# Kernel tuning notes

Hardware: AMD Instinct MI355X
Metric: run time of the kernel (lower is better)

Reference implementation:

```python
import jax, jax.numpy as jnp
import numpy as np

B, S, C, H = 2, 4096, 512, 8
D = C // H  # per-head depth


def setup_inputs() -> dict:
    key = jax.random.key(0)
    ks = jax.random.split(key, 12)
    scale = 1.0 / np.sqrt(C)
    inp = {
        "q": jax.random.normal(ks[0], (B, S, C), jnp.float32),
        "k": jax.random.normal(ks[1], (B, S, C), jnp.float32),
        "v": jax.random.normal(ks[2], (B, S, C), jnp.float32),
        "mask": jax.random.randint(ks[3], (1, 1, S, S), 0, 2).astype(jnp.float32),
        "wq": jax.random.normal(ks[4], (C, C), jnp.float32) * scale,
        "bq": jnp.zeros((C,), jnp.float32),
        "wk": jax.random.normal(ks[5], (C, C), jnp.float32) * scale,
        "bk": jnp.zeros((C,), jnp.float32),
        "wv": jax.random.normal(ks[6], (C, C), jnp.float32) * scale,
        "bv": jnp.zeros((C,), jnp.float32),
        "wo": jax.random.normal(ks[7], (C, C), jnp.float32) * scale,
        "bo": jnp.zeros((C,), jnp.float32),
    }
    return inp


def _split_heads(x):
    # [B,S,C] -> [B,H,S,D]
    b, s, _ = x.shape
    return x.reshape(b, s, H, D).transpose(0, 2, 1, 3)


def reference(q, k, v, mask, wq, bq, wk, bk, wv, bv, wo, bo):
    # torch Linear: y = x @ W.T + b
    qh = _split_heads(q @ wq.T + bq)  # [B,H,S,D]
    kh = _split_heads(k @ wk.T + bk)
    vh = _split_heads(v @ wv.T + bv)

    # scaled dot-product attention with additive legacy mask
    scores = jnp.einsum("bhqd,bhkd->bhqk", qh, kh) / jnp.sqrt(jnp.float32(D))
    scores = scores + mask * jnp.float32(-1e12)
    attn = jax.nn.softmax(scores, axis=-1)  # [B,H,Sq,Sk]
    out_h = jnp.einsum("bhqk,bhkd->bhqd", attn, vh)  # [B,H,S,D]

    # merge heads and output projection
    concat = out_h.transpose(0, 2, 1, 3).reshape(q.shape[0], -1, C)
    out = concat @ wo.T + bo  # [B,S,C]
    return out, attn
```

## Files before the change

### kernel.cpp

```cpp
#include <hip/hip_runtime.h>
#include <hip/hip_bf16.h>
#include <cstdint>

#define SB 4096
#define CB 512
#define HB 8
#define DB 64
#define BB 2

#define QSCALE 0.18033688011112042f

typedef __attribute__((ext_vector_type(8))) short s16x8;
typedef __attribute__((ext_vector_type(4))) short s16x4;
typedef __attribute__((ext_vector_type(4))) float f32x4;

__device__ __forceinline__ short f2bf(float f) {
    union { float f; unsigned int u; } v; v.f = f;
    unsigned int r = v.u + 0x7fffu + ((v.u >> 16) & 1u);
    return (short)(r >> 16);
}

__device__ __forceinline__ unsigned int cvtpk(float lo, float hi) {
    unsigned int r;
    asm("v_cvt_pk_bf16_f32 %0, %1, %2" : "=v"(r) : "v"(lo), "v"(hi));
    return r;
}

__device__ __forceinline__ f32x4 mfma16(s16x8 a, s16x8 b, f32x4 c) {
    return __builtin_amdgcn_mfma_f32_16x16x32_bf16(a, b, c, 0, 0, 0);
}

__device__ __forceinline__ f32x4 mfma16x16(s16x4 a, s16x4 b, f32x4 c) {
    asm("v_mfma_f32_16x16x16_bf16 %0, %1, %2, %0" : "+v"(c) : "v"(a), "v"(b));
    return c;
}

__global__ __launch_bounds__(256) void qkv_proj_kernel(
    const float* __restrict__ q, const float* __restrict__ k, const float* __restrict__ v,
    const float* __restrict__ wq, const float* __restrict__ wk, const float* __restrict__ wv,
    const float* __restrict__ bq, const float* __restrict__ bk, const float* __restrict__ bv,
    unsigned short* __restrict__ Qh, unsigned short* __restrict__ Kh,
    unsigned short* __restrict__ Vt)
{
    const int z = blockIdx.z;
    const float* X = (z == 0) ? q : (z == 1) ? k : v;
    const float* W = (z == 0) ? wq : (z == 1) ? wk : wv;
    const float* bias = (z == 0) ? bq : (z == 1) ? bk : bv;
    unsigned short* dst = (z == 0) ? Qh : (z == 1) ? Kh : Vt;
    const float oscale = (z == 0) ? QSCALE : 1.0f;
    const int which = (z == 2) ? 2 : 0;

    __shared__ __align__(16) short As[128 * 40];
    __shared__ __align__(16) short Bs[64 * 40];
    const int t = threadIdx.x;
    const int w = t >> 6, lane = t & 63, g = lane >> 4, c = lane & 15;
    const int wr = w >> 1, wc = w & 1;
    const int m0 = blockIdx.x * 128, n0 = blockIdx.y * 64;

    f32x4 acc[4][2];
#pragma unroll
    for (int i = 0; i < 4; ++i)
#pragma unroll
        for (int j = 0; j < 2; ++j) acc[i][j] = (f32x4){0.f, 0.f, 0.f, 0.f};

    for (int k0 = 0; k0 < CB; k0 += 32) {
        __syncthreads();
#pragma unroll
        for (int i = 0; i < 4; ++i) {
            int idx = t + i * 256; int r = idx >> 3, c4 = idx & 7;
            float4 vv = *(const float4*)(X + (size_t)(m0 + r) * CB + k0 + c4 * 4);
            s16x4 p; p[0] = f2bf(vv.x); p[1] = f2bf(vv.y); p[2] = f2bf(vv.z); p[3] = f2bf(vv.w);
            *(s16x4*)&As[r * 40 + c4 * 4] = p;
        }
#pragma unroll
        for (int i = 0; i < 2; ++i) {
            int idx = t + i * 256; int r = idx >> 3, c4 = idx & 7;
            float4 vv = *(const float4*)(W + (size_t)(n0 + r) * CB + k0 + c4 * 4);
            s16x4 p; p[0] = f2bf(vv.x); p[1] = f2bf(vv.y); p[2] = f2bf(vv.z); p[3] = f2bf(vv.w);
            *(s16x4*)&Bs[r * 40 + c4 * 4] = p;
        }
        __syncthreads();
        const int koff = g * 8;
        s16x8 a[4], bb[2];
#pragma unroll
        for (int mf = 0; mf < 4; ++mf)
            a[mf] = *(const s16x8*)&As[(wr * 64 + mf * 16 + c) * 40 + koff];
#pragma unroll
        for (int nf = 0; nf < 2; ++nf)
            bb[nf] = *(const s16x8*)&Bs[(wc * 32 + nf * 16 + c) * 40 + koff];
#pragma unroll
        for (int mf = 0; mf < 4; ++mf)
#pragma unroll
            for (int nf = 0; nf < 2; ++nf)
                acc[mf][nf] = mfma16(a[mf], bb[nf], acc[mf][nf]);
    }

#pragma unroll
    for (int nf = 0; nf < 2; ++nf) {
        const int n = n0 + wc * 32 + nf * 16 + c;
        const float bv2 = bias[n];
        const int h = n >> 6, d = n & 63;
#pragma unroll
        for (int mf = 0; mf < 4; ++mf) {
#pragma unroll
            for (int r = 0; r < 4; ++r) {
                int m = m0 + wr * 64 + mf * 16 + g * 4 + r;
                float val = (acc[mf][nf][r] + bv2) * oscale;
                int b = m >> 12, s = m & (SB - 1);
                size_t off;
                if (which == 0) off = (((size_t)(b * HB + h)) * SB + s) * DB + d;
                else            off = (((size_t)(b * HB + h)) * DB + d) * SB + s;
                dst[off] = (unsigned short)f2bf(val);
            }
        }
    }
}

__global__ __launch_bounds__(256) void maskbits_kernel(
    const float* __restrict__ mask, unsigned long long* __restrict__ bits)
{
    size_t idx = (size_t)blockIdx.x * 256 + threadIdx.x;
    float v = mask[idx];
    unsigned long long b = __ballot(v != 0.0f);
    if ((threadIdx.x & 63) == 0) bits[idx >> 6] = b;
}

__global__ __launch_bounds__(512) void flash_kernel(
    const unsigned short* __restrict__ Qh, const unsigned short* __restrict__ Kh,
    const unsigned short* __restrict__ Vt, const unsigned long long* __restrict__ mbits,
    unsigned short* __restrict__ concat, float* __restrict__ invbuf)
{
    __shared__ __align__(16) short Klds[2][64 * 64];
    __shared__ __align__(16) short Vlds[2][64 * 64];

    const int t = threadIdx.x, w = t >> 6, lane = t & 63, g = lane >> 4, c = lane & 15;
    const int bid = blockIdx.x;
    const int xcd = bid & 7, idx = bid >> 3;
    const int bh = xcd * 2 + (idx >> 5);
    const int qb = idx & 31;
    const int b = bh >> 3, h = bh & 7;
    const int i0 = qb * 128;

    const unsigned short* Qbase = Qh + ((size_t)bh * SB + i0 + w * 16) * DB;
    const unsigned short* Kbase = Kh + (size_t)bh * SB * DB;
    const unsigned short* Vbase = Vt + (size_t)bh * DB * SB;

    s16x8 qf[2];
#pragma unroll
    for (int ks = 0; ks < 2; ++ks)
        qf[ks] = *(const s16x8*)(Qbase + (size_t)c * DB + ks * 32 + g * 8);

    const int qrow = i0 + w * 16 + c;
    const size_t mrowbase = (size_t)qrow * (SB / 64);
    float rowacc = 0.f;
    f32x4 acc[4];
#pragma unroll
    for (int df = 0; df < 4; ++df) acc[df] = (f32x4){0.f, 0.f, 0.f, 0.f};

    const int sr = t >> 3;
    const int colb = (t & 7) * 16;
    const int swz = (sr & 7) << 4;

    s16x8 kreg, vreg;

    auto LOAD = [&](int j0) {
        kreg = *(const s16x8*)((const char*)(Kbase + (size_t)(j0 + sr) * DB) + colb);
        vreg = *(const s16x8*)((const char*)(Vbase + (size_t)sr * SB + j0) + colb);
    };
    auto STORE = [&](int buf) {
        *(s16x8*)((char*)&Klds[buf][0] + sr * 128 + (colb ^ swz)) = kreg;
        *(s16x8*)((char*)&Vlds[buf][0] + sr * 128 + (colb ^ swz)) = vreg;
    };
    auto COMPUTE = [&](int buf, unsigned long long mw64) {
        f32x4 sc[4];
        __builtin_amdgcn_s_setprio(1);
#pragma unroll
        for (int jf = 0; jf < 4; ++jf) {
            sc[jf] = (f32x4){0.f, 0.f, 0.f, 0.f};
#pragma unroll
            for (int ks = 0; ks < 2; ++ks) {
                s16x8 kf = *(const s16x8*)((char*)&Klds[buf][0] + (jf * 16 + c) * 128 +
                                           ((ks * 64 + g * 16) ^ ((c & 7) << 4)));
                sc[jf] = mfma16(kf, qf[ks], sc[jf]);
            }
        }
        __builtin_amdgcn_s_setprio(0);

        const unsigned long long mw = mw64 >> (g * 4);
        const unsigned int nib[4] = {
            (unsigned int)mw & 0xFu, (unsigned int)(mw >> 16) & 0xFu,
            (unsigned int)(mw >> 32) & 0xFu, (unsigned int)(mw >> 48) & 0xFu };

        s16x4 pf4[4];
#pragma unroll
        for (int jf = 0; jf < 4; ++jf) {
            float e[4];
#pragma unroll
            for (int r = 0; r < 4; ++r)
                e[r] = ((nib[jf] >> r) & 1u) ? 0.f : __builtin_amdgcn_exp2f(sc[jf][r]);
            rowacc += (e[0] + e[1]) + (e[2] + e[3]);
            union { unsigned int u[2]; s16x4 v; } pk;
            pk.u[0] = cvtpk(e[0], e[1]);
            pk.u[1] = cvtpk(e[2], e[3]);
            pf4[jf] = pk.v;
        }

        __builtin_amdgcn_s_setprio(1);
#pragma unroll
        for (int df = 0; df < 4; ++df) {
#pragma unroll
            for (int jf = 0; jf < 4; ++jf) {
                s16x4 vf = *(const s16x4*)((char*)&Vlds[buf][0] + (df * 16 + c) * 128 +
                                           ((jf * 32 + g * 8) ^ ((c & 7) << 4)));
                acc[df] = mfma16x16(pf4[jf], vf, acc[df]);
            }
        }
        __builtin_amdgcn_s_setprio(0);
    };

    unsigned long long mwcur = mbits[mrowbase];
    LOAD(0);
    STORE(0);
    __syncthreads();
    int cur = 0;
    for (int jt = 0; jt < SB / 64 - 1; ++jt) {
        LOAD((jt + 1) * 64);
        unsigned long long mwnext = mbits[mrowbase + jt + 1];
        COMPUTE(cur, mwcur);
        STORE(cur ^ 1);
        __syncthreads();
        mwcur = mwnext;
        cur ^= 1;
    }
    COMPUTE(cur, mwcur);

    rowacc += __shfl_xor(rowacc, 16);
    rowacc += __shfl_xor(rowacc, 32);
    const float inv = 1.0f / rowacc;
    if (lane < 16) invbuf[(size_t)bh * SB + i0 + w * 16 + c] = inv;

    float ir[4];
#pragma unroll
    for (int r = 0; r < 4; ++r) ir[r] = __shfl(inv, g * 4 + r);

#pragma unroll
    for (int df = 0; df < 4; ++df) {
#pragma unroll
        for (int r = 0; r < 4; ++r) {
            const int s_ = i0 + w * 16 + g * 4 + r;
            concat[(size_t)(b * SB + s_) * CB + h * DB + df * 16 + c] =
                (unsigned short)f2bf(acc[df][r] * ir[r]);
        }
    }
}

__global__ __launch_bounds__(256) void attn_write_kernel(
    const unsigned short* __restrict__ Qh, const unsigned short* __restrict__ Kh,
    const unsigned long long* __restrict__ mbits, const float* __restrict__ invbuf,
    float* __restrict__ attnO)
{
    __shared__ __align__(16) float TP[4][16 * 64];

    const int t = threadIdx.x, w = t >> 6, lane = t & 63, g = lane >> 4, c = lane & 15;
    const int q0 = blockIdx.x * 64;
    const int ks0 = blockIdx.y * 512 + w * 128;
    const size_t bh = blockIdx.z;
    const unsigned short* Qb_ = Qh + (bh * SB + q0) * DB;
    const unsigned short* Kb_ = Kh + bh * SB * DB;
    float* aO = attnO + bh * (size_t)SB * SB;
    char* tp = (char*)&TP[w][0];

    s16x8 qf[4][2];
    float invv[4];
    size_t mrb[4];
#pragma unroll
    for (int qi = 0; qi < 4; ++qi) {
#pragma unroll
        for (int ks = 0; ks < 2; ++ks)
            qf[qi][ks] = *(const s16x8*)(Qb_ + (size_t)(qi * 16 + c) * DB + ks * 32 + g * 8);
        invv[qi] = invbuf[bh * SB + q0 + qi * 16 + c];
        mrb[qi] = (size_t)(q0 + qi * 16 + c) * (SB / 64);
    }

#pragma unroll
    for (int kc = 0; kc < 2; ++kc) {
        const int kch = ks0 + kc * 64;
        s16x8 kf[4][2];
#pragma unroll
        for (int jf = 0; jf < 4; ++jf)
#pragma unroll
            for (int ks = 0; ks < 2; ++ks)
                kf[jf][ks] = *(const s16x8*)(Kb_ + (size_t)(kch + jf * 16 + c) * DB + ks * 32 + g * 8);

#pragma unroll
        for (int qi = 0; qi < 4; ++qi) {
            f32x4 sc[4];
#pragma unroll
            for (int jf = 0; jf < 4; ++jf) {
                sc[jf] = (f32x4){0.f, 0.f, 0.f, 0.f};
#pragma unroll
                for (int ks = 0; ks < 2; ++ks)
                    sc[jf] = mfma16(kf[jf][ks], qf[qi][ks], sc[jf]);
            }
            unsigned long long mw = mbits[mrb[qi] + (kch >> 6)] >> (g * 4);
            const unsigned int nib[4] = {
                (unsigned int)mw & 0xFu, (unsigned int)(mw >> 16) & 0xFu,
                (unsigned int)(mw >> 32) & 0xFu, (unsigned int)(mw >> 48) & 0xFu };
            const float iv = invv[qi];

#pragma unroll
            for (int jf = 0; jf < 4; ++jf) {
                f32x4 o;
#pragma unroll
                for (int r = 0; r < 4; ++r)
                    o[r] = ((nib[jf] >> r) & 1u) ? 0.f : __builtin_amdgcn_exp2f(sc[jf][r]) * iv;
                *(f32x4*)(tp + c * 256 + ((jf * 64 + g * 16) ^ (c << 4))) = o;
            }

            const size_t gbase = (size_t)(q0 + qi * 16) * SB + kch;
#pragma unroll
            for (int i = 0; i < 4; ++i) {
                const int rr = i * 4 + g;
                f32x4 vv = *(const f32x4*)(tp + rr * 256 + ((c * 16) ^ (rr << 4)));
                __builtin_nontemporal_store(vv, (f32x4*)(aO + gbase + (size_t)rr * SB + c * 4));
            }
        }
    }
}

__global__ __launch_bounds__(256) void final_kernel(
    const unsigned short* __restrict__ Ain, const float* __restrict__ W,
    const float* __restrict__ bias, float* __restrict__ out)
{
    __shared__ __align__(16) short As[128 * 40];
    __shared__ __align__(16) short Bs[64 * 40];
    const int t = threadIdx.x;
    const int w = t >> 6, lane = t & 63, g = lane >> 4, c = lane & 15;
    const int wr = w >> 1, wc = w & 1;
    const int m0 = blockIdx.x * 128, n0 = blockIdx.y * 64;

    f32x4 acc[4][2];
#pragma unroll
    for (int i = 0; i < 4; ++i)
#pragma unroll
        for (int j = 0; j < 2; ++j) acc[i][j] = (f32x4){0.f, 0.f, 0.f, 0.f};

    for (int k0 = 0; k0 < CB; k0 += 32) {
        __syncthreads();
#pragma unroll
        for (int i = 0; i < 2; ++i) {
            int idx = t + i * 256; int r = idx >> 2, ch = idx & 3;
            *(s16x8*)&As[r * 40 + ch * 8] =
                *(const s16x8*)(Ain + (size_t)(m0 + r) * CB + k0 + ch * 8);
        }
#pragma unroll
        for (int i = 0; i < 2; ++i) {
            int idx = t + i * 256; int r = idx >> 3, c4 = idx & 7;
            float4 v = *(const float4*)(W + (size_t)(n0 + r) * CB + k0 + c4 * 4);
            s16x4 p; p[0] = f2bf(v.x); p[1] = f2bf(v.y); p[2] = f2bf(v.z); p[3] = f2bf(v.w);
            *(s16x4*)&Bs[r * 40 + c4 * 4] = p;
        }
        __syncthreads();
        const int koff = g * 8;
        s16x8 a[4], bb[2];
#pragma unroll
        for (int mf = 0; mf < 4; ++mf)
            a[mf] = *(const s16x8*)&As[(wr * 64 + mf * 16 + c) * 40 + koff];
#pragma unroll
        for (int nf = 0; nf < 2; ++nf)
            bb[nf] = *(const s16x8*)&Bs[(wc * 32 + nf * 16 + c) * 40 + koff];
#pragma unroll
        for (int mf = 0; mf < 4; ++mf)
#pragma unroll
            for (int nf = 0; nf < 2; ++nf)
                acc[mf][nf] = mfma16(a[mf], bb[nf], acc[mf][nf]);
    }

#pragma unroll
    for (int nf = 0; nf < 2; ++nf) {
        const int n = n0 + wc * 32 + nf * 16 + c;
        const float bv = bias[n];
#pragma unroll
        for (int mf = 0; mf < 4; ++mf) {
#pragma unroll
            for (int r = 0; r < 4; ++r) {
                int m = m0 + wr * 64 + mf * 16 + g * 4 + r;
                out[(size_t)m * CB + n] = acc[mf][nf][r] + bv;
            }
        }
    }
}

extern "C" void kernel_launch(void* const* d_in, const int* in_sizes, int n_in,
                              void* d_out, int out_size, void* d_ws, size_t ws_size,
                              hipStream_t stream) {
    const float* q    = (const float*)d_in[0];
    const float* k    = (const float*)d_in[1];
    const float* v    = (const float*)d_in[2];
    const float* mask = (const float*)d_in[3];
    const float* wq   = (const float*)d_in[4];
    const float* bq   = (const float*)d_in[5];
    const float* wk   = (const float*)d_in[6];
    const float* bk   = (const float*)d_in[7];
    const float* wv   = (const float*)d_in[8];
    const float* bv   = (const float*)d_in[9];
    const float* wo   = (const float*)d_in[10];
    const float* bo   = (const float*)d_in[11];

    const size_t NE = (size_t)BB * HB * SB * DB;
    unsigned short* Qh     = (unsigned short*)d_ws;
    unsigned short* Kh     = Qh + NE;
    unsigned short* Vt     = Kh + NE;
    unsigned short* concat = Vt + NE;
    unsigned long long* mbits = (unsigned long long*)((char*)d_ws + 4 * NE * sizeof(unsigned short));
    float* invbuf = (float*)((char*)d_ws + 4 * NE * sizeof(unsigned short) + (size_t)SB * SB / 8);

    float* outp  = (float*)d_out;
    float* attnp = outp + (size_t)BB * SB * CB;

    qkv_proj_kernel<<<dim3(64, 8, 3), 256, 0, stream>>>(q, k, v, wq, wk, wv, bq, bk, bv,
                                                        Qh, Kh, Vt);
    maskbits_kernel<<<dim3((SB * SB) / 256, 1, 1), 256, 0, stream>>>(mask, mbits);
    flash_kernel<<<dim3(512, 1, 1), 512, 0, stream>>>(Qh, Kh, Vt, mbits, concat, invbuf);
    final_kernel<<<dim3(64, 8, 1), 256, 0, stream>>>(concat, wo, bo, outp);
    attn_write_kernel<<<dim3(SB / 64, 8, HB * BB), 256, 0, stream>>>(Qh, Kh, mbits, invbuf, attnp);
}
```

Before: 434.9 us.

## Merge mask packing into QKV launch and output projection into attention write

Folds the mask-bit packing kernel into the QKV projection launch as extra z-slices, and folds the output projection GEMM into the attention-probability write kernel as an extra z-slice. This cuts the launch count from five to three, and lets independent work share the GPU at the same time. It also removes the s_setprio hints in the flash kernel and switches the large attention-matrix stores from nontemporal to regular stores. That could change cache behavior for the 512MB attention output.

Measured after the change: 485.4 us. +11.6%, slower.

```diff
diff --git a/kernel.cpp b/kernel.cpp
--- a/kernel.cpp
+++ b/kernel.cpp
@@ -35,14 +35,24 @@
     return c;
 }
 
-__global__ __launch_bounds__(256) void qkv_proj_kernel(
+__global__ __launch_bounds__(256) void qkv_mask_kernel(
     const float* __restrict__ q, const float* __restrict__ k, const float* __restrict__ v,
     const float* __restrict__ wq, const float* __restrict__ wk, const float* __restrict__ wv,
     const float* __restrict__ bq, const float* __restrict__ bk, const float* __restrict__ bv,
     unsigned short* __restrict__ Qh, unsigned short* __restrict__ Kh,
-    unsigned short* __restrict__ Vt)
+    unsigned short* __restrict__ Vt,
+    const float* __restrict__ mask, unsigned long long* __restrict__ bits)
 {
     const int z = blockIdx.z;
+    if (z >= 3) {
+        size_t idx = (((size_t)(z - 3) * 512) + blockIdx.y * 64 + blockIdx.x) * 256
+                     + threadIdx.x;
+        float mv = mask[idx];
+        unsigned long long bmask = __ballot(mv != 0.0f);
+        if ((threadIdx.x & 63) == 0) bits[idx >> 6] = bmask;
+        return;
+    }
+
     const float* X = (z == 0) ? q : (z == 1) ? k : v;
     const float* W = (z == 0) ? wq : (z == 1) ? wk : wv;
     const float* bias = (z == 0) ? bq : (z == 1) ? bk : bv;
@@ -114,15 +124,6 @@
             }
         }
     }
-}
-
-__global__ __launch_bounds__(256) void maskbits_kernel(
-    const float* __restrict__ mask, unsigned long long* __restrict__ bits)
-{
-    size_t idx = (size_t)blockIdx.x * 256 + threadIdx.x;
-    float v = mask[idx];
-    unsigned long long b = __ballot(v != 0.0f);
-    if ((threadIdx.x & 63) == 0) bits[idx >> 6] = b;
 }
 
 __global__ __launch_bounds__(512) void flash_kernel(
@@ -173,7 +174,6 @@
     };
     auto COMPUTE = [&](int buf, unsigned long long mw64) {
         f32x4 sc[4];
-        __builtin_amdgcn_s_setprio(1);
 #pragma unroll
         for (int jf = 0; jf < 4; ++jf) {
             sc[jf] = (f32x4){0.f, 0.f, 0.f, 0.f};
@@ -184,7 +184,6 @@
                 sc[jf] = mfma16(kf, qf[ks], sc[jf]);
             }
         }
-        __builtin_amdgcn_s_setprio(0);
 
         const unsigned long long mw = mw64 >> (g * 4);
         const unsigned int nib[4] = {
@@ -205,7 +204,6 @@
             pf4[jf] = pk.v;
         }
 
-        __builtin_amdgcn_s_setprio(1);
 #pragma unroll
         for (int df = 0; df < 4; ++df) {
 #pragma unroll
@@ -215,7 +213,6 @@
                 acc[df] = mfma16x16(pf4[jf], vf, acc[df]);
             }
         }
-        __builtin_amdgcn_s_setprio(0);
     };
 
     unsigned long long mwcur = mbits[mrowbase];
@@ -254,11 +251,74 @@
     }
 }
 
-__global__ __launch_bounds__(256) void attn_write_kernel(
+__global__ __launch_bounds__(256) void attn_final_kernel(
     const unsigned short* __restrict__ Qh, const unsigned short* __restrict__ Kh,
     const unsigned long long* __restrict__ mbits, const float* __restrict__ invbuf,
-    float* __restrict__ attnO)
+    float* __restrict__ attnO,
+    const unsigned short* __restrict__ Ain, const float* __restrict__ W,
+    const float* __restrict__ bias, float* __restrict__ out)
 {
+    if (blockIdx.z == 16) {
+        __shared__ __align__(16) short As[128 * 40];
+        __shared__ __align__(16) short Bs[64 * 40];
+        const int t = threadIdx.x;
+        const int w = t >> 6, lane = t & 63, g = lane >> 4, c = lane & 15;
+        const int wr = w >> 1, wc = w & 1;
+        const int m0 = blockIdx.x * 128, n0 = blockIdx.y * 64;
+
+        f32x4 acc[4][2];
+#pragma unroll
+        for (int i = 0; i < 4; ++i)
+#pragma unroll
+            for (int j = 0; j < 2; ++j) acc[i][j] = (f32x4){0.f, 0.f, 0.f, 0.f};
+
+        for (int k0 = 0; k0 < CB; k0 += 32) {
+            __syncthreads();
+#pragma unroll
+            for (int i = 0; i < 2; ++i) {
+                int idx = t + i * 256; int r = idx >> 2, ch = idx & 3;
+                *(s16x8*)&As[r * 40 + ch * 8] =
+                    *(const s16x8*)(Ain + (size_t)(m0 + r) * CB + k0 + ch * 8);
+            }
+#pragma unroll
+            for (int i = 0; i < 2; ++i) {
+                int idx = t + i * 256; int r = idx >> 3, c4 = idx & 7;
+                float4 v = *(const float4*)(W + (size_t)(n0 + r) * CB + k0 + c4 * 4);
+                s16x4 p; p[0] = f2bf(v.x); p[1] = f2bf(v.y); p[2] = f2bf(v.z); p[3] = f2bf(v.w);
+                *(s16x4*)&Bs[r * 40 + c4 * 4] = p;
+            }
+            __syncthreads();
+            const int koff = g * 8;
+            s16x8 a[4], bb[2];
+#pragma unroll
+            for (int mf = 0; mf < 4; ++mf)
+                a[mf] = *(const s16x8*)&As[(wr * 64 + mf * 16 + c) * 40 + koff];
+#pragma unroll
+            for (int nf = 0; nf < 2; ++nf)
+                bb[nf] = *(const s16x8*)&Bs[(wc * 32 + nf * 16 + c) * 40 + koff];
+#pragma unroll
+            for (int mf = 0; mf < 4; ++mf)
+#pragma unroll
+                for (int nf = 0; nf < 2; ++nf)
+                    acc[mf][nf] = mfma16(a[mf], bb[nf], acc[mf][nf]);
+        }
+
+#pragma unroll
+        for (int nf = 0; nf < 2; ++nf) {
+            const int n = n0 + wc * 32 + nf * 16 + c;
+            const float bv = bias[n];
+#pragma unroll
+            for (int mf = 0; mf < 4; ++mf) {
+#pragma unroll
+                for (int r = 0; r < 4; ++r) {
+                    int m = m0 + wr * 64 + mf * 16 + g * 4 + r;
+                    out[(size_t)m * CB + n] = acc[mf][nf][r] + bv;
+                }
+            }
+        }
+        return;
+    }
+
     __shared__ __align__(16) float TP[4][16 * 64];
 
     const int t = threadIdx.x, w = t >> 6, lane = t & 63, g = lane >> 4, c = lane & 15;
@@ -322,70 +382,7 @@
             for (int i = 0; i < 4; ++i) {
                 const int rr = i * 4 + g;
                 f32x4 vv = *(const f32x4*)(tp + rr * 256 + ((c * 16) ^ (rr << 4)));
-                __builtin_nontemporal_store(vv, (f32x4*)(aO + gbase + (size_t)rr * SB + c * 4));
-            }
-        }
-    }
-}
-
-__global__ __launch_bounds__(256) void final_kernel(
-    const unsigned short* __restrict__ Ain, const float* __restrict__ W,
-    const float* __restrict__ bias, float* __restrict__ out)
-{
-    __shared__ __align__(16) short As[128 * 40];
-    __shared__ __align__(16) short Bs[64 * 40];
-    const int t = threadIdx.x;
-    const int w = t >> 6, lane = t & 63, g = lane >> 4, c = lane & 15;
-    const int wr = w >> 1, wc = w & 1;
-    const int m0 = blockIdx.x * 128, n0 = blockIdx.y * 64;
-
-    f32x4 acc[4][2];
-#pragma unroll
-    for (int i = 0; i < 4; ++i)
-#pragma unroll
-        for (int j = 0; j < 2; ++j) acc[i][j] = (f32x4){0.f, 0.f, 0.f, 0.f};
-
-    for (int k0 = 0; k0 < CB; k0 += 32) {
-        __syncthreads();
-#pragma unroll
-        for (int i = 0; i < 2; ++i) {
-            int idx = t + i * 256; int r = idx >> 2, ch = idx & 3;
-            *(s16x8*)&As[r * 40 + ch * 8] =
-                *(const s16x8*)(Ain + (size_t)(m0 + r) * CB + k0 + ch * 8);
-        }
-#pragma unroll
-        for (int i = 0; i < 2; ++i) {
-            int idx = t + i * 256; int r = idx >> 3, c4 = idx & 7;
-            float4 v = *(const float4*)(W + (size_t)(n0 + r) * CB + k0 + c4 * 4);
-            s16x4 p; p[0] = f2bf(v.x); p[1] = f2bf(v.y); p[2] = f2bf(v.z); p[3] = f2bf(v.w);
-            *(s16x4*)&Bs[r * 40 + c4 * 4] = p;
-        }
-        __syncthreads();
-        const int koff = g * 8;
-        s16x8 a[4], bb[2];
-#pragma unroll
-        for (int mf = 0; mf < 4; ++mf)
-            a[mf] = *(const s16x8*)&As[(wr * 64 + mf * 16 + c) * 40 + koff];
-#pragma unroll
-        for (int nf = 0; nf < 2; ++nf)
-            bb[nf] = *(const s16x8*)&Bs[(wc * 32 + nf * 16 + c) * 40 + koff];
-#pragma unroll
-        for (int mf = 0; mf < 4; ++mf)
-#pragma unroll
-            for (int nf = 0; nf < 2; ++nf)
-                acc[mf][nf] = mfma16(a[mf], bb[nf], acc[mf][nf]);
-    }
-
-#pragma unroll
-    for (int nf = 0; nf < 2; ++nf) {
-        const int n = n0 + wc * 32 + nf * 16 + c;
-        const float bv = bias[n];
-#pragma unroll
-        for (int mf = 0; mf < 4; ++mf) {
-#pragma unroll
-            for (int r = 0; r < 4; ++r) {
-                int m = m0 + wr * 64 + mf * 16 + g * 4 + r;
-                out[(size_t)m * CB + n] = acc[mf][nf][r] + bv;
+                *(f32x4*)(aO + gbase + (size_t)rr * SB + c * 4) = vv;
             }
         }
     }
@@ -418,10 +415,9 @@
     float* outp  = (float*)d_out;
     float* attnp = outp + (size_t)BB * SB * CB;
 
-    qkv_proj_kernel<<<dim3(64, 8, 3), 256, 0, stream>>>(q, k, v, wq, wk, wv, bq, bk, bv,
-                                                        Qh, Kh, Vt);
-    maskbits_kernel<<<dim3((SB * SB) / 256, 1, 1), 256, 0, stream>>>(mask, mbits);
+    qkv_mask_kernel<<<dim3(64, 8, 131), 256, 0, stream>>>(
+        q, k, v, wq, wk, wv, bq, bk, bv, Qh, Kh, Vt, mask, mbits);
     flash_kernel<<<dim3(512, 1, 1), 512, 0, stream>>>(Qh, Kh, Vt, mbits, concat, invbuf);
-    final_kernel<<<dim3(64, 8, 1), 256, 0, stream>>>(concat, wo, bo, outp);
-    attn_write_kernel<<<dim3(SB / 64, 8, HB * BB), 256, 0, stream>>>(Qh, Kh, mbits, invbuf, attnp);
-}
+    attn_final_kernel<<<dim3(SB / 64, 8, HB * BB + 1), 256, 0, stream>>>(
+        Qh, Kh, mbits, invbuf, attnp, concat, wo, bo, outp);
+}
```
